# Optimization experiments

Hardware: AMD Instinct MI355X
Metric: run time of the kernel (lower is better)

## Reference

```python
import jax, jax.numpy as jnp
import numpy as np

D = 1024
EPS = 1e-5


def layer_norm(x, w, b):
    mu = jnp.mean(x, axis=-1, keepdims=True)
    var = jnp.var(x, axis=-1, keepdims=True)
    return (x - mu) * jax.lax.rsqrt(var + EPS) * w + b


def setup_inputs() -> dict:
    key = jax.random.key(0)
    ks = jax.random.split(key, 8)
    B, S = 8, 2048
    s_attn = 1.0 / np.sqrt(D)
    s_fc = 1.0 / np.sqrt(D)
    s_proj = 1.0 / np.sqrt(4 * D)
    return {
        "x": jax.random.normal(ks[0], (B, S, D), dtype=jnp.float32),
        "ln1_w": jnp.ones((D,), jnp.float32),
        "ln1_b": jnp.zeros((D,), jnp.float32),
        "W_attn": jax.random.uniform(ks[1], (D, 3 * D), jnp.float32, -s_attn, s_attn),
        "b_attn": jax.random.uniform(ks[2], (3 * D,), jnp.float32, -s_attn, s_attn),
        "ln2_w": jnp.ones((D,), jnp.float32),
        "ln2_b": jnp.zeros((D,), jnp.float32),
        "W_fc": jax.random.uniform(ks[3], (D, 4 * D), jnp.float32, -s_fc, s_fc),
        "b_fc": jax.random.uniform(ks[4], (4 * D,), jnp.float32, -s_fc, s_fc),
        "W_proj": jax.random.uniform(ks[5], (4 * D, D), jnp.float32, -s_proj, s_proj),
        "b_proj": jax.random.uniform(ks[6], (D,), jnp.float32, -s_proj, s_proj),
    }


def reference(x, ln1_w, ln1_b, W_attn, b_attn, ln2_w, ln2_b, W_fc, b_fc, W_proj, b_proj):
    # Attention sub-block (single-head, hand-rolled)
    h = layer_norm(x, ln1_w, ln1_b)                       # [B,S,D]
    qkv = h @ W_attn + b_attn                              # [B,S,3D]
    q, k, v = jnp.split(qkv, 3, axis=2)
    scores = jnp.einsum('bsd,btd->bst', q, k) / jnp.sqrt(jnp.float32(D))
    attn = jax.nn.softmax(scores, axis=-1)                 # [B,S,S]
    x = x + jnp.einsum('bst,btd->bsd', attn, v)            # residual
    # MLP sub-block (no residual in original)
    h = layer_norm(x, ln2_w, ln2_b)
    h = jax.nn.gelu(h @ W_fc + b_fc, approximate=False)    # torch GELU default = erf
    return h @ W_proj + b_proj
```

## Files before the change

kernel.cpp:

```cpp
#include <hip/hip_runtime.h>
#include <hip/hip_bf16.h>
#include <math.h>

#define D_MODEL 1024
#define SEQ 2048
#define BATCH 8

typedef unsigned short u16;
typedef __attribute__((ext_vector_type(8))) short bf16x8;
typedef __attribute__((ext_vector_type(4))) float f32x4;

__device__ inline u16 f2bf(float f) {
  __hip_bfloat16 h = __float2bfloat16(f);
  return __builtin_bit_cast(u16, h);
}
__device__ inline float bf2f(u16 u) {
  return __builtin_bit_cast(float, (unsigned)u << 16);
}

__device__ __forceinline__ void async_cp16(const u16* g, u16* l) {
  __builtin_amdgcn_global_load_lds(
      (const __attribute__((address_space(1))) void*)g,
      (__attribute__((address_space(3))) void*)l, 16, 0, 0);
}

__global__ __launch_bounds__(256) void ln_kernel(
    const float* __restrict__ x, const float* __restrict__ w,
    const float* __restrict__ b, u16* __restrict__ out) {
  int row = blockIdx.x;
  int t = threadIdx.x;
  const float4* xr = (const float4*)(x + (size_t)row * D_MODEL);
  float4 v = xr[t];
  float s = v.x + v.y + v.z + v.w;
  float s2 = v.x * v.x + v.y * v.y + v.z * v.z + v.w * v.w;
  for (int o = 32; o > 0; o >>= 1) {
    s += __shfl_down(s, o);
    s2 += __shfl_down(s2, o);
  }
  __shared__ float red[10];
  int wave = t >> 6, lane = t & 63;
  if (lane == 0) { red[wave] = s; red[4 + wave] = s2; }
  __syncthreads();
  if (t == 0) {
    float S = red[0] + red[1] + red[2] + red[3];
    float S2 = red[4] + red[5] + red[6] + red[7];
    float mu = S * (1.f / D_MODEL);
    float var = S2 * (1.f / D_MODEL) - mu * mu;
    red[8] = mu;
    red[9] = rsqrtf(var + 1e-5f);
  }
  __syncthreads();
  float mu = red[8], rstd = red[9];
  float4 w4 = ((const float4*)w)[t];
  float4 b4 = ((const float4*)b)[t];
  ushort4 o4;
  o4.x = f2bf((v.x - mu) * rstd * w4.x + b4.x);
  o4.y = f2bf((v.y - mu) * rstd * w4.y + b4.y);
  o4.z = f2bf((v.z - mu) * rstd * w4.z + b4.z);
  o4.w = f2bf((v.w - mu) * rstd * w4.w + b4.w);
  ((ushort4*)(out + (size_t)row * D_MODEL))[t] = o4;
}

__global__ __launch_bounds__(256) void softmax_bf16_kernel(u16* __restrict__ p) {
  int row = blockIdx.x;
  int t = threadIdx.x;
  int4 q = ((const int4*)(p + (size_t)row * SEQ))[t];
  u16 us[8];
  __builtin_memcpy(us, &q, 16);
  float vals[8];
  for (int i = 0; i < 8; i++) vals[i] = bf2f(us[i]);
  float m = vals[0];
  for (int i = 1; i < 8; i++) m = fmaxf(m, vals[i]);
  for (int o = 32; o > 0; o >>= 1) m = fmaxf(m, __shfl_down(m, o));
  __shared__ float red[6];
  int wave = t >> 6, lane = t & 63;
  if (lane == 0) red[wave] = m;
  __syncthreads();
  if (t == 0) red[4] = fmaxf(fmaxf(red[0], red[1]), fmaxf(red[2], red[3]));
  __syncthreads();
  m = red[4];
  float s = 0.f;
  for (int i = 0; i < 8; i++) { vals[i] = __expf(vals[i] - m); s += vals[i]; }
  for (int o = 32; o > 0; o >>= 1) s += __shfl_down(s, o);
  if (lane == 0) red[wave] = s;
  __syncthreads();
  if (t == 0) red[5] = red[0] + red[1] + red[2] + red[3];
  __syncthreads();
  float inv = 1.f / red[5];
  union { u16 us[8]; int4 v4; } pk;
  for (int i = 0; i < 8; i++) pk.us[i] = f2bf(vals[i] * inv);
  ((int4*)(p + (size_t)row * SEQ))[t] = pk.v4;
}

__global__ __launch_bounds__(256) void wconv_t(
    const float* __restrict__ W, u16* __restrict__ Wt, int K, int N) {
  int k0 = blockIdx.x * 64, n0 = blockIdx.y * 64;
  __shared__ u16 tile[64][65];
  int t = threadIdx.x;
  for (int p = 0; p < 16; p++) {
    int idx = p * 256 + t;
    int r = idx >> 6, c = idx & 63;
    tile[r][c] = f2bf(W[(size_t)(k0 + r) * N + n0 + c]);
  }
  __syncthreads();
  for (int p = 0; p < 16; p++) {
    int idx = p * 256 + t;
    int r = idx >> 6, c = idx & 63;
    Wt[(size_t)(n0 + r) * K + k0 + c] = tile[c][r];
  }
}

enum { EPI_QKV = 0, EPI_SCALE_BF16 = 1, EPI_RESID_F32 = 2,
       EPI_GELU_BF16 = 3, EPI_BIAS_F32 = 4 };

template <int EPI>
__global__ __launch_bounds__(256, 4) void gemm_bt(
    const u16* __restrict__ A, const u16* __restrict__ Bt,
    void* __restrict__ Cv, const float* __restrict__ bias,
    const float* __restrict__ resid, u16* __restrict__ vTp,
    int M, int N, int K, int lda, int ldb, int ldc, float scale,
    long long saB, long long sbB, long long scB, long long srB) {
  __shared__ __align__(16) u16 lA[128 * 64];
  __shared__ __align__(16) u16 lB[128 * 64];
  int t = threadIdx.x;
  int zb = blockIdx.z;
  A += (size_t)zb * saB;
  Bt += (size_t)zb * sbB;

  int gx = gridDim.x;
  int flat = blockIdx.x + gx * blockIdx.y;
  int rem = flat % (4 * gx);
  int m0 = ((flat / (4 * gx)) * 4 + (rem & 3)) * 128;
  int n0 = (rem >> 2) * 128;

  int wv = t >> 6, lane = t & 63;

  int srow = t >> 3;
  int scg = (t & 7) ^ ((t >> 3) & 7);
  int scol = scg << 3;
  const u16* gA = A + (size_t)(m0 + srow) * lda + scol;
  const u16* gB = Bt + (size_t)(n0 + srow) * ldb + scol;
  u16* lAd = lA + t * 8;
  u16* lBd = lB + t * 8;

  int wm = (wv >> 1) * 64, wn = (wv & 1) * 64;
  int lr = lane & 15, lq = lane >> 4;
  int keyr = lr & 7;
  f32x4 acc[4][4] = {};

  for (int k0 = 0; k0 < K; k0 += 64) {
    #pragma unroll
    for (int r = 0; r < 4; r++) {
      async_cp16(gA + (size_t)(r * 32) * lda, lAd + r * 2048);
      async_cp16(gB + (size_t)(r * 32) * ldb, lBd + r * 2048);
    }
    gA += 64; gB += 64;
    __syncthreads();
    #pragma unroll
    for (int ks = 0; ks < 2; ks++) {
      bf16x8 af[4], bfr[4];
      #pragma unroll
      for (int i = 0; i < 4; i++)
        af[i] = *(const bf16x8*)(lA + (wm + i * 16 + lr) * 64 +
                                 (((lq + 4 * ks) ^ keyr) << 3));
      #pragma unroll
      for (int j = 0; j < 4; j++)
        bfr[j] = *(const bf16x8*)(lB + (wn + j * 16 + lr) * 64 +
                                  (((lq + 4 * ks) ^ keyr) << 3));
      #pragma unroll
      for (int i = 0; i < 4; i++)
        #pragma unroll
        for (int j = 0; j < 4; j++)
          acc[i][j] = __builtin_amdgcn_mfma_f32_16x16x32_bf16(
              af[i], bfr[j], acc[i][j], 0, 0, 0);
    }
    __syncthreads();
  }

  float* Cf = (float*)Cv + (size_t)zb * scB;
  u16* Ch = (u16*)Cv + (size_t)zb * scB;
  const float* rz = resid + (size_t)zb * srB;

  if constexpr (EPI == EPI_QKV) {
    if (n0 >= 2048) {
      for (int i = 0; i < 4; i++) {
        int row0 = m0 + wm + i * 16 + lq * 4;
        int batch = row0 >> 11, s0 = row0 & 2047;
        for (int j = 0; j < 4; j++) {
          int d = n0 - 2048 + wn + j * 16 + lr;
          float bcol = bias[n0 + wn + j * 16 + lr];
          ushort4 o4;
          o4.x = f2bf(acc[i][j][0] + bcol);
          o4.y = f2bf(acc[i][j][1] + bcol);
          o4.z = f2bf(acc[i][j][2] + bcol);
          o4.w = f2bf(acc[i][j][3] + bcol);
          *(ushort4*)(vTp + (((size_t)batch * 1024 + d) << 11) + s0) = o4;
        }
      }
      return;
    }
  }

  for (int i = 0; i < 4; i++) {
    for (int j = 0; j < 4; j++) {
      int col = n0 + wn + j * 16 + lr;
      float bcol = (EPI == EPI_QKV || EPI == EPI_GELU_BF16 ||
                    EPI == EPI_BIAS_F32) ? bias[col] : 0.f;
      for (int r = 0; r < 4; r++) {
        int row = m0 + wm + i * 16 + lq * 4 + r;
        float v = acc[i][j][r];
        size_t off = (size_t)row * ldc + col;
        if constexpr (EPI == EPI_QKV) {
          Ch[off] = f2bf(v + bcol);
        } else if constexpr (EPI == EPI_SCALE_BF16) {
          Ch[off] = f2bf(v * scale);
        } else if constexpr (EPI == EPI_RESID_F32) {
          Cf[off] = v + rz[off];
        } else if constexpr (EPI == EPI_GELU_BF16) {
          float xx = v + bcol;
          float u = xx * (0.7978845608f + 0.0356774081f * xx * xx);
          float e = __expf(2.f * u);
          float th = 1.f - 2.f * __builtin_amdgcn_rcpf(e + 1.f);
          Ch[off] = f2bf(0.5f * xx * (1.f + th));
        } else {
          Cf[off] = v + bcol;
        }
      }
    }
  }
}

#define PHB() __builtin_amdgcn_s_barrier()

#define LDA_(t_, ks_, fi_) \
  (*(const bf16x8*)(lds + (((t_) & 1) * 4 + (ks_)) * 8192 + aoff + (fi_) * 512))
#define LDB_(t_, ks_, fj_) \
  (*(const bf16x8*)(lds + (((t_) & 1) * 4 + 2 + (ks_)) * 8192 + boff + (fj_) * 512))

#define MMQ(base_) do {                                               \
    __builtin_amdgcn_s_setprio(1);                                    \
    _Pragma("unroll")                                                 \
    for (int ii = 0; ii < 4; ii++)                                    \
      _Pragma("unroll")                                               \
      for (int jj = 0; jj < 4; jj++)                                  \
        acc[(base_) + ii][jj] = __builtin_amdgcn_mfma_f32_16x16x32_bf16( \
            a_[ii], b_[jj], acc[(base_) + ii][jj], 0, 0, 0);          \
    __builtin_amdgcn_s_setprio(0); } while (0)

template <int EPI>
__global__ __launch_bounds__(512, 2) void gemm256(
    const u16* __restrict__ A, const u16* __restrict__ Bt,
    void* __restrict__ Cv, const float* __restrict__ bias,
    const float* __restrict__ resid, u16* __restrict__ vTp,
    int M, int N, int K, int lda, int ldb, int ldc, float scale,
    long long saB, long long sbB, long long scB, long long srB) {
  __shared__ __align__(16) u16 lds[65536];
  int t = threadIdx.x;
  int zb = blockIdx.z;
  A += (size_t)zb * saB;
  Bt += (size_t)zb * sbB;

  int gx = gridDim.x;
  int nwg = gx * gridDim.y;
  int flat = blockIdx.x + gx * blockIdx.y;
  int swz = flat;
  if (!(nwg & 7)) { int cpx = nwg >> 3; swz = (flat & 7) * cpx + (flat >> 3); }
  int mt = swz / gx, nt = swz % gx;
  int m0 = mt * 256, n0 = nt * 256;

  int wv = t >> 6, lane = t & 63, lr = lane & 15, lq = lane >> 4;
  int wm = (wv >> 2) * 128, wn = (wv & 3) * 64;
  int pg8 = (lq ^ ((lr >> 1) & 3)) << 3;
  int aoff = (wm + lr) * 32 + pg8;
  int boff = (wn + lr) * 32 + pg8;

  int r0 = t >> 2, r1 = r0 + 128;
  int c0 = ((t & 3) ^ ((r0 >> 1) & 3)) << 3;
  const u16* gA0 = A + (size_t)(m0 + r0) * lda + c0;
  const u16* gA1 = A + (size_t)(m0 + r1) * lda + c0;
  const u16* gB0 = Bt + (size_t)(n0 + r0) * ldb + c0;
  const u16* gB1 = Bt + (size_t)(n0 + r1) * ldb + c0;

  f32x4 acc[8][4] = {};
  int NT = K >> 6, NI = NT >> 1;

  auto stage = [&](int tile, int ab, int ks) {
    int ko = tile * 64 + ks * 32;
    u16* d = lds + ((tile & 1) * 4 + ab * 2 + ks) * 8192 + t * 8;
    if (ab) {
      async_cp16(gB0 + ko, d);
      async_cp16(gB1 + ko, d + 4096);
    } else {
      async_cp16(gA0 + ko, d);
      async_cp16(gA1 + ko, d + 4096);
    }
  };

  stage(0, 0, 0); stage(0, 1, 0); stage(0, 0, 1); stage(0, 1, 1);
  stage(1, 0, 0); stage(1, 1, 0);
  asm volatile("s_waitcnt vmcnt(8)" ::: "memory");
  PHB();

  bf16x8 a_[4], b_[4];
  for (int it = 0; it < NI; it++) {
    int ta = 2 * it, tb = ta + 1, tc = ta + 2, td = ta + 3;
    bool ck = tc < NT, dk = td < NT;
    bool last = (it == NI - 1);

    #pragma unroll
    for (int f = 0; f < 4; f++) a_[f] = LDA_(ta, 0, f);
    #pragma unroll
    for (int f = 0; f < 4; f++) b_[f] = LDB_(ta, 0, f);
    stage(tb, 0, 1);
    PHB();
    MMQ(0);
    PHB();

    #pragma unroll
    for (int f = 0; f < 4; f++) a_[f] = LDA_(ta, 0, 4 + f);
    stage(tb, 1, 1);
    PHB();
    MMQ(4);
    asm volatile("s_waitcnt vmcnt(8)" ::: "memory");
    PHB();

    #pragma unroll
    for (int f = 0; f < 4; f++) a_[f] = LDA_(ta, 1, f);
    #pragma unroll
    for (int f = 0; f < 4; f++) b_[f] = LDB_(ta, 1, f);
    if (ck) stage(tc, 0, 0);
    PHB();
    MMQ(0);
    PHB();

    #pragma unroll
    for (int f = 0; f < 4; f++) a_[f] = LDA_(ta, 1, 4 + f);
    if (ck) stage(tc, 1, 0);
    PHB();
    MMQ(4);
    if (last) { asm volatile("s_waitcnt vmcnt(4)" ::: "memory"); }
    else      { asm volatile("s_waitcnt vmcnt(8)" ::: "memory"); }
    PHB();

    #pragma unroll
    for (int f = 0; f < 4; f++) a_[f] = LDA_(tb, 0, f);
    #pragma unroll
    for (int f = 0; f < 4; f++) b_[f] = LDB_(tb, 0, f);
    if (ck) stage(tc, 0, 1);
    PHB();
    MMQ(0);
    PHB();

    #pragma unroll
    for (int f = 0; f < 4; f++) a_[f] = LDA_(tb, 0, 4 + f);
    if (ck) stage(tc, 1, 1);
    PHB();
    MMQ(4);
    if (last) { asm volatile("s_waitcnt vmcnt(0)" ::: "memory"); }
    else      { asm volatile("s_waitcnt vmcnt(8)" ::: "memory"); }
    PHB();

    #pragma unroll
    for (int f = 0; f < 4; f++) a_[f] = LDA_(tb, 1, f);
    #pragma unroll
    for (int f = 0; f < 4; f++) b_[f] = LDB_(tb, 1, f);
    if (dk) stage(td, 0, 0);
    PHB();
    MMQ(0);
    PHB();

    #pragma unroll
    for (int f = 0; f < 4; f++) a_[f] = LDA_(tb, 1, 4 + f);
    if (dk) stage(td, 1, 0);
    PHB();
    MMQ(4);
    asm volatile("s_waitcnt vmcnt(8)" ::: "memory");
    PHB();
  }

  float* Cf = (float*)Cv + (size_t)zb * scB;
  u16* Ch = (u16*)Cv + (size_t)zb * scB;
  const float* rz = resid + (size_t)zb * srB;

  if constexpr (EPI == EPI_QKV) {
    if (n0 >= 2048) {
      #pragma unroll
      for (int i = 0; i < 8; i++) {
        int row0 = m0 + wm + i * 16 + lq * 4;
        int batch = row0 >> 11, s0 = row0 & 2047;
        #pragma unroll
        for (int j = 0; j < 4; j++) {
          int d = n0 - 2048 + wn + j * 16 + lr;
          float bcol = bias[n0 + wn + j * 16 + lr];
          ushort4 o4;
          o4.x = f2bf(acc[i][j][0] + bcol);
          o4.y = f2bf(acc[i][j][1] + bcol);
          o4.z = f2bf(acc[i][j][2] + bcol);
          o4.w = f2bf(acc[i][j][3] + bcol);
          *(ushort4*)(vTp + (((size_t)batch * 1024 + d) << 11) + s0) = o4;
        }
      }
      return;
    }
  }

  for (int i = 0; i < 8; i++) {
    for (int j = 0; j < 4; j++) {
      int col = n0 + wn + j * 16 + lr;
      float bcol = (EPI == EPI_QKV || EPI == EPI_GELU_BF16 ||
                    EPI == EPI_BIAS_F32) ? bias[col] : 0.f;
      for (int r = 0; r < 4; r++) {
        int row = m0 + wm + i * 16 + lq * 4 + r;
        float v = acc[i][j][r];
        size_t off = (size_t)row * ldc + col;
        if constexpr (EPI == EPI_QKV) {
          Ch[off] = f2bf(v + bcol);
        } else if constexpr (EPI == EPI_SCALE_BF16) {
          Ch[off] = f2bf(v * scale);
        } else if constexpr (EPI == EPI_RESID_F32) {
          Cf[off] = v + rz[off];
        } else if constexpr (EPI == EPI_GELU_BF16) {
          float xx = v + bcol;
          float u = xx * (0.7978845608f + 0.0356774081f * xx * xx);
          float e = __expf(2.f * u);
          float th = 1.f - 2.f * __builtin_amdgcn_rcpf(e + 1.f);
          Ch[off] = f2bf(0.5f * xx * (1.f + th));
        } else {
          Cf[off] = v + bcol;
        }
      }
    }
  }
}

extern "C" void kernel_launch(void* const* d_in, const int* in_sizes, int n_in,
                              void* d_out, int out_size, void* d_ws, size_t ws_size,
                              hipStream_t stream) {
  const float* x      = (const float*)d_in[0];
  const float* ln1_w  = (const float*)d_in[1];
  const float* ln1_b  = (const float*)d_in[2];
  const float* W_attn = (const float*)d_in[3];
  const float* b_attn = (const float*)d_in[4];
  const float* ln2_w  = (const float*)d_in[5];
  const float* ln2_b  = (const float*)d_in[6];
  const float* W_fc   = (const float*)d_in[7];
  const float* b_fc   = (const float*)d_in[8];
  const float* W_proj = (const float*)d_in[9];
  const float* b_proj = (const float*)d_in[10];
  float* out = (float*)d_out;

  if (ws_size < 190840832ull) return;
  char* ws = (char*)d_ws;
  u16* hb   = (u16*)(ws + 0);
  u16* qk   = (u16*)(ws + 33554432ull);
  u16* vT   = (u16*)(ws + 100663296ull);
  u16* sc   = (u16*)(ws + 134217728ull);
  u16* fc   = (u16*)(ws + 33554432ull);
  u16* WaT  = (u16*)(ws + 167772160ull);
  u16* WfT  = (u16*)(ws + 174063616ull);
  u16* WpT  = (u16*)(ws + 182452224ull);

  wconv_t<<<dim3(1024 / 64, 3072 / 64), 256, 0, stream>>>(W_attn, WaT, 1024, 3072);
  wconv_t<<<dim3(1024 / 64, 4096 / 64), 256, 0, stream>>>(W_fc, WfT, 1024, 4096);
  wconv_t<<<dim3(4096 / 64, 1024 / 64), 256, 0, stream>>>(W_proj, WpT, 4096, 1024);

  ln_kernel<<<BATCH * SEQ, 256, 0, stream>>>(x, ln1_w, ln1_b, hb);

  gemm256<EPI_QKV><<<dim3(12, 64, 1), 512, 0, stream>>>(
      hb, WaT, qk, b_attn, x, vT, BATCH * SEQ, 3072, 1024, 1024, 1024, 2048, 1.f,
      0, 0, 0, 0);

  const float iss = 0.03125f;
  for (int c = 0; c < 2; c++) {
    const u16* qb = qk + (size_t)c * 4 * SEQ * 2048;
    gemm256<EPI_SCALE_BF16><<<dim3(8, 8, 4), 512, 0, stream>>>(
        qb, qb + 1024, sc, nullptr, x, nullptr, SEQ, SEQ, 1024, 2048, 2048, SEQ,
        iss, (long long)SEQ * 2048, (long long)SEQ * 2048, (long long)SEQ * SEQ, 0);
    softmax_bf16_kernel<<<4 * SEQ, 256, 0, stream>>>(sc);
    gemm_bt<EPI_RESID_F32><<<dim3(8, 16, 4), 256, 0, stream>>>(
        sc, vT + (size_t)c * 4 * D_MODEL * SEQ,
        out + (size_t)c * 4 * SEQ * D_MODEL, nullptr,
        x + (size_t)c * 4 * SEQ * D_MODEL, nullptr, SEQ, D_MODEL, SEQ,
        SEQ, SEQ, D_MODEL, 1.f,
        (long long)SEQ * SEQ, (long long)D_MODEL * SEQ,
        (long long)SEQ * D_MODEL, (long long)SEQ * D_MODEL);
  }

  ln_kernel<<<BATCH * SEQ, 256, 0, stream>>>(out, ln2_w, ln2_b, hb);

  gemm256<EPI_GELU_BF16><<<dim3(16, 64, 1), 512, 0, stream>>>(
      hb, WfT, fc, b_fc, x, nullptr, BATCH * SEQ, 4096, 1024, 1024, 1024, 4096,
      1.f, 0, 0, 0, 0);

  gemm256<EPI_BIAS_F32><<<dim3(4, 64, 1), 512, 0, stream>>>(
      fc, WpT, out, b_proj, x, nullptr, BATCH * SEQ, 1024, 4096, 4096, 4096,
      1024, 1.f, 0, 0, 0, 0);
}
```

Before: 771.6 us.

## Double-buffer GEMM register fragments so LDS reads overlap MFMA

Replaces the single a_/b_ register fragment set with two ping-pong sets (aA/aB, bA/bB). Each phase now loads the next fragments from LDS while MFMAs run on the current ones, and the first fragments of the next tile are prefetched before the loop iteration ends. This cuts the barriers per phase from two to one and retunes the vmcnt waits. The cost is higher register pressure under launch_bounds(512,2). The reordered barriers and waits also risk LDS read/write hazards, for example the tb,0 B fragments being read after the tc,1,0 stage is issued.

```diff
diff --git a/kernel.cpp b/kernel.cpp
--- a/kernel.cpp
+++ b/kernel.cpp
@@ -230,22 +230,22 @@
   }
 }
 
-#define PHB() __builtin_amdgcn_s_barrier()
-
 #define LDA_(t_, ks_, fi_) \
   (*(const bf16x8*)(lds + (((t_) & 1) * 4 + (ks_)) * 8192 + aoff + (fi_) * 512))
 #define LDB_(t_, ks_, fj_) \
   (*(const bf16x8*)(lds + (((t_) & 1) * 4 + 2 + (ks_)) * 8192 + boff + (fj_) * 512))
 
-#define MMQ(base_) do {                                               \
+#define MMQ2(base_, aF_, bF_) do {                                    \
     __builtin_amdgcn_s_setprio(1);                                    \
     _Pragma("unroll")                                                 \
     for (int ii = 0; ii < 4; ii++)                                    \
       _Pragma("unroll")                                               \
       for (int jj = 0; jj < 4; jj++)                                  \
         acc[(base_) + ii][jj] = __builtin_amdgcn_mfma_f32_16x16x32_bf16( \
-            a_[ii], b_[jj], acc[(base_) + ii][jj], 0, 0, 0);          \
+            aF_[ii], bF_[jj], acc[(base_) + ii][jj], 0, 0, 0);        \
     __builtin_amdgcn_s_setprio(0); } while (0)
+
+#define BAR() __builtin_amdgcn_s_barrier()
 
 template <int EPI>
 __global__ __launch_bounds__(512, 2) void gemm256(
@@ -299,83 +299,82 @@
   stage(0, 0, 0); stage(0, 1, 0); stage(0, 0, 1); stage(0, 1, 1);
   stage(1, 0, 0); stage(1, 1, 0);
   asm volatile("s_waitcnt vmcnt(8)" ::: "memory");
-  PHB();
-
-  bf16x8 a_[4], b_[4];
+  BAR();
+
+  bf16x8 aA[4], aB[4], bA[4], bB[4];
+  #pragma unroll
+  for (int f = 0; f < 4; f++) aA[f] = LDA_(0, 0, f);
+  #pragma unroll
+  for (int f = 0; f < 4; f++) bA[f] = LDB_(0, 0, f);
+
   for (int it = 0; it < NI; it++) {
     int ta = 2 * it, tb = ta + 1, tc = ta + 2, td = ta + 3;
     bool ck = tc < NT, dk = td < NT;
     bool last = (it == NI - 1);
 
     #pragma unroll
-    for (int f = 0; f < 4; f++) a_[f] = LDA_(ta, 0, f);
-    #pragma unroll
-    for (int f = 0; f < 4; f++) b_[f] = LDB_(ta, 0, f);
+    for (int f = 0; f < 4; f++) aB[f] = LDA_(ta, 0, 4 + f);
     stage(tb, 0, 1);
-    PHB();
-    MMQ(0);
-    PHB();
-
-    #pragma unroll
-    for (int f = 0; f < 4; f++) a_[f] = LDA_(ta, 0, 4 + f);
+    MMQ2(0, aA, bA);
+    asm volatile("s_waitcnt vmcnt(6)" ::: "memory");
+    BAR();
+
+    #pragma unroll
+    for (int f = 0; f < 4; f++) aA[f] = LDA_(ta, 1, f);
+    #pragma unroll
+    for (int f = 0; f < 4; f++) bB[f] = LDB_(ta, 1, f);
     stage(tb, 1, 1);
-    PHB();
-    MMQ(4);
-    asm volatile("s_waitcnt vmcnt(8)" ::: "memory");
-    PHB();
-
-    #pragma unroll
-    for (int f = 0; f < 4; f++) a_[f] = LDA_(ta, 1, f);
-    #pragma unroll
-    for (int f = 0; f < 4; f++) b_[f] = LDB_(ta, 1, f);
+    MMQ2(4, aB, bA);
+    BAR();
+
+    #pragma unroll
+    for (int f = 0; f < 4; f++) aB[f] = LDA_(ta, 1, 4 + f);
     if (ck) stage(tc, 0, 0);
-    PHB();
-    MMQ(0);
-    PHB();
-
-    #pragma unroll
-    for (int f = 0; f < 4; f++) a_[f] = LDA_(ta, 1, 4 + f);
+    MMQ2(0, aA, bB);
+    if (last) { asm volatile("s_waitcnt vmcnt(4)" ::: "memory"); }
+    else      { asm volatile("s_waitcnt vmcnt(6)" ::: "memory"); }
+    BAR();
+
+    #pragma unroll
+    for (int f = 0; f < 4; f++) aA[f] = LDA_(tb, 0, f);
+    #pragma unroll
+    for (int f = 0; f < 4; f++) bA[f] = LDB_(tb, 0, f);
     if (ck) stage(tc, 1, 0);
-    PHB();
-    MMQ(4);
-    if (last) { asm volatile("s_waitcnt vmcnt(4)" ::: "memory"); }
-    else      { asm volatile("s_waitcnt vmcnt(8)" ::: "memory"); }
-    PHB();
-
-    #pragma unroll
-    for (int f = 0; f < 4; f++) a_[f] = LDA_(tb, 0, f);
-    #pragma unroll
-    for (int f = 0; f < 4; f++) b_[f] = LDB_(tb, 0, f);
+    MMQ2(4, aB, bB);
+    BAR();
+
+    #pragma unroll
+    for (int f = 0; f < 4; f++) aB[f] = LDA_(tb, 0, 4 + f);
     if (ck) stage(tc, 0, 1);
-    PHB();
-    MMQ(0);
-    PHB();
-
-    #pragma unroll
-    for (int f = 0; f < 4; f++) a_[f] = LDA_(tb, 0, 4 + f);
+    MMQ2(0, aA, bA);
+    if (last) { asm volatile("s_waitcnt vmcnt(0)" ::: "memory"); }
+    else      { asm volatile("s_waitcnt vmcnt(6)" ::: "memory"); }
+    BAR();
+
+    #pragma unroll
+    for (int f = 0; f < 4; f++) aA[f] = LDA_(tb, 1, f);
+    #pragma unroll
+    for (int f = 0; f < 4; f++) bB[f] = LDB_(tb, 1, f);
     if (ck) stage(tc, 1, 1);
-    PHB();
-    MMQ(4);
-    if (last) { asm volatile("s_waitcnt vmcnt(0)" ::: "memory"); }
-    else      { asm volatile("s_waitcnt vmcnt(8)" ::: "memory"); }
-    PHB();
-
-    #pragma unroll
-    for (int f = 0; f < 4; f++) a_[f] = LDA_(tb, 1, f);
-    #pragma unroll
-    for (int f = 0; f < 4; f++) b_[f] = LDB_(tb, 1, f);
+    MMQ2(4, aB, bA);
+    BAR();
+
+    #pragma unroll
+    for (int f = 0; f < 4; f++) aB[f] = LDA_(tb, 1, 4 + f);
     if (dk) stage(td, 0, 0);
-    PHB();
-    MMQ(0);
-    PHB();
-
-    #pragma unroll
-    for (int f = 0; f < 4; f++) a_[f] = LDA_(tb, 1, 4 + f);
+    MMQ2(0, aA, bB);
+    asm volatile("s_waitcnt vmcnt(6)" ::: "memory");
+    BAR();
+
+    if (!last) {
+      #pragma unroll
+      for (int f = 0; f < 4; f++) aA[f] = LDA_(tc, 0, f);
+      #pragma unroll
+      for (int f = 0; f < 4; f++) bA[f] = LDB_(tc, 0, f);
+    }
     if (dk) stage(td, 1, 0);
-    PHB();
-    MMQ(4);
-    asm volatile("s_waitcnt vmcnt(8)" ::: "memory");
-    PHB();
+    MMQ2(4, aB, bB);
+    BAR();
   }
 
   float* Cf = (float*)Cv + (size_t)zb * scB;
```

Measured after the change: 1.012 ms. +31.2%, slower.
